# Kernel tuning notes

Hardware: AMD Instinct MI355X
Metric: run time of the kernel (lower is better)

The kernel has to match this reference:

```python
import jax, jax.numpy as jnp
import numpy as np

DIM = 640
HEADS = 10
HEAD_DIM = DIM // HEADS
SCALE = DIM ** (-0.5)  # note: module scales by full dim**-0.5, not head_dim


def setup_inputs() -> dict:
    key = jax.random.key(0)
    ks = jax.random.split(key, 5)
    B, N = 16, 1024
    x = jax.random.normal(ks[0], (B, N, DIM), dtype=jnp.float32)
    w_qkv = jax.random.normal(ks[1], (DIM, 3 * DIM), dtype=jnp.float32) * (DIM ** -0.5)
    b_qkv = jnp.zeros((3 * DIM,), dtype=jnp.float32)
    w_out = jax.random.normal(ks[2], (DIM, DIM), dtype=jnp.float32) * (DIM ** -0.5)
    b_out = jnp.zeros((DIM,), dtype=jnp.float32)
    return {"x": x, "w_qkv": w_qkv, "b_qkv": b_qkv, "w_out": w_out, "b_out": b_out}


def reference(x, w_qkv, b_qkv, w_out, b_out):
    B, N, _ = x.shape
    qkv = x @ w_qkv + b_qkv                     # [B, N, 3*DIM]
    qkv = qkv.reshape(B, N, 3, HEADS, HEAD_DIM)
    q, k, v = qkv[:, :, 0], qkv[:, :, 1], qkv[:, :, 2]   # [B, N, H, Dh]
    # scores: QK^T scaled by dim**-0.5 (module's normfactor)
    scores = jnp.einsum('bihd,bjhd->bhij', q, k) * SCALE  # [B, H, N, N]
    attn = jax.nn.softmax(scores, axis=-1)
    out = jnp.einsum('bhij,bjhd->bihd', attn, v)          # [B, N, H, Dh]
    out = out.reshape(B, N, DIM)
    return out @ w_out + b_out
```

## Files before the change

### kernel.cpp

```cpp
#include <hip/hip_runtime.h>

#define DIM 640
#define NHEADS 10
#define HDIM 64
#define SEQ 1024
#define BATCH 16
#define MROWS (BATCH * SEQ)
#define QKVN (3 * DIM)
#define NBH (BATCH * NHEADS)

typedef float f32x4 __attribute__((ext_vector_type(4)));
typedef __bf16 bf16x8 __attribute__((ext_vector_type(8)));
typedef short s16x4 __attribute__((ext_vector_type(4)));

#define SM_C 0.057027536f

__device__ __forceinline__ unsigned short f2b(float f) {
  union { __bf16 h; unsigned short u; } v;
  v.h = (__bf16)f;
  return v.u;
}

__device__ __forceinline__ f32x4 mfma16(bf16x8 a, bf16x8 b, f32x4 c) {
  return __builtin_amdgcn_mfma_f32_16x16x32_bf16(a, b, c, 0, 0, 0);
}
__device__ __forceinline__ f32x4 mfma1k(s16x4 a, s16x4 b, f32x4 c) {
  return __builtin_amdgcn_mfma_f32_16x16x16bf16_1k(a, b, c, 0, 0, 0);
}

typedef __attribute__((address_space(3))) unsigned int as3_u32;
typedef const __attribute__((address_space(1))) unsigned int as1_u32;
__device__ __forceinline__ void glds16(const unsigned short* g, unsigned short* l) {
  __builtin_amdgcn_global_load_lds((as1_u32*)g, (as3_u32*)l, 16, 0, 0);
}

__global__ __launch_bounds__(256) void convert_x(
    const float* __restrict__ X, unsigned short* __restrict__ xb) {
  int i = (blockIdx.x * 256 + threadIdx.x) * 4;
  float4 v = *(const float4*)(X + i);
  ushort4 s;
  s.x = f2b(v.x); s.y = f2b(v.y); s.z = f2b(v.z); s.w = f2b(v.w);
  *(ushort4*)(xb + i) = s;
}

__global__ __launch_bounds__(256) void transpose_w(
    const float* __restrict__ W, unsigned short* __restrict__ Wt, int R, int C) {
  __shared__ int tile[32][33];
  const int tx = threadIdx.x & 31, ty = threadIdx.x >> 5;
  const int c0 = blockIdx.x * 32, r0 = blockIdx.y * 32;
#pragma unroll
  for (int i = 0; i < 4; ++i)
    tile[ty + 8 * i][tx] = f2b(W[(r0 + ty + 8 * i) * C + c0 + tx]);
  __syncthreads();
#pragma unroll
  for (int i = 0; i < 4; ++i)
    Wt[(c0 + ty + 8 * i) * R + r0 + tx] = (unsigned short)tile[tx][ty + 8 * i];
}

__global__ __launch_bounds__(256) void qkv_gemm(
    const unsigned short* __restrict__ A, const unsigned short* __restrict__ Bt,
    const float* __restrict__ bias,
    unsigned short* __restrict__ qw, unsigned short* __restrict__ kw,
    unsigned short* __restrict__ vtw) {
  __shared__ __attribute__((aligned(16))) unsigned short As[128 * 64];
  __shared__ __attribute__((aligned(16))) unsigned short Bs[128 * 64];
  const int t = threadIdx.x;
  const int lane = t & 63, w = t >> 6;
  const int quad = lane >> 4, cl = lane & 15;
  const int m0 = blockIdx.y * 128, n0 = blockIdx.x * 128;
  const int wr = (w >> 1) * 64, wc = (w & 1) * 64;

  const int r8 = lane >> 3;
  const int sw = ((lane & 7) ^ r8) * 8;
  const unsigned short* asrc = A + (size_t)(m0 + w * 32 + r8) * DIM + sw;
  const unsigned short* bsrc = Bt + (size_t)(n0 + w * 32 + r8) * DIM + sw;

  const int x = cl & 7;
  const int aoff0 = (wr + cl) * 64 + (quad ^ x) * 8;
  const int aoff1 = (wr + cl) * 64 + ((4 + quad) ^ x) * 8;
  const int boff0 = (wc + cl) * 64 + (quad ^ x) * 8;
  const int boff1 = (wc + cl) * 64 + ((4 + quad) ^ x) * 8;

  f32x4 acc[4][4];
#pragma unroll
  for (int i = 0; i < 4; ++i)
#pragma unroll
    for (int j = 0; j < 4; ++j) acc[i][j] = (f32x4){0.f, 0.f, 0.f, 0.f};

  for (int kt = 0; kt < DIM / 64; ++kt) {
    __syncthreads();
#pragma unroll
    for (int i = 0; i < 4; ++i) {
      glds16(asrc + (size_t)i * 8 * DIM, &As[(w * 32 + i * 8) * 64]);
      glds16(bsrc + (size_t)i * 8 * DIM, &Bs[(w * 32 + i * 8) * 64]);
    }
    asrc += 64; bsrc += 64;
    __syncthreads();
#pragma unroll
    for (int ks = 0; ks < 2; ++ks) {
      const int ao = ks ? aoff1 : aoff0, bo = ks ? boff1 : boff0;
      bf16x8 af[4], bfr[4];
#pragma unroll
      for (int i = 0; i < 4; ++i) af[i] = *(const bf16x8*)&As[ao + i * 1024];
#pragma unroll
      for (int j = 0; j < 4; ++j) bfr[j] = *(const bf16x8*)&Bs[bo + j * 1024];
#pragma unroll
      for (int i = 0; i < 4; ++i)
#pragma unroll
        for (int j = 0; j < 4; ++j) acc[i][j] = mfma16(af[i], bfr[j], acc[i][j]);
    }
  }

  const int sec = n0 / DIM;
  unsigned short* qk = (sec == 0) ? qw : kw;
  const float sc = (sec == 0) ? SM_C : 1.0f;
#pragma unroll
  for (int j = 0; j < 4; ++j) {
    int cc = n0 + wc + j * 16 + cl;
    int cr = cc - sec * DIM;
    int h = cr >> 6, d = cr & 63;
    float bv = bias[cc];
#pragma unroll
    for (int i = 0; i < 4; ++i) {
      int rbase = m0 + wr + i * 16 + quad * 4;
      int b = rbase >> 10, n = rbase & 1023;
      int bh = b * NHEADS + h;
      if (sec < 2) {
        size_t base = ((size_t)bh * SEQ + n) * HDIM + d;
#pragma unroll
        for (int r = 0; r < 4; ++r)
          qk[base + (size_t)r * HDIM] = f2b((acc[i][j][r] + bv) * sc);
      } else {
        ushort4 s;
        s.x = f2b(acc[i][j][0] + bv);
        s.y = f2b(acc[i][j][1] + bv);
        s.z = f2b(acc[i][j][2] + bv);
        s.w = f2b(acc[i][j][3] + bv);
        *(ushort4*)(vtw + ((size_t)bh * HDIM + d) * SEQ + n) = s;
      }
    }
  }
}

__global__ __launch_bounds__(256) void attn_kernel(
    const unsigned short* __restrict__ qw, const unsigned short* __restrict__ kw,
    const unsigned short* __restrict__ vtw, unsigned short* __restrict__ out) {
  __shared__ __attribute__((aligned(16))) unsigned short Ks[2][64 * 64];
  __shared__ __attribute__((aligned(16))) unsigned short Vs[2][64 * 64];
  const int t = threadIdx.x;
  const int lane = t & 63, w = t >> 6;
  const int quad = lane >> 4, cl = lane & 15;
  const int flat = blockIdx.x;
  const int bh = flat % NBH;
  const int qb = flat / NBH;
  const size_t qkbase = (size_t)bh * SEQ * HDIM;
  const size_t vbase  = (size_t)bh * HDIM * SEQ;

  const int r8 = lane >> 3;
  const int sw = ((lane & 7) ^ r8) * 8;
  const unsigned short* ksrc = kw + qkbase + (size_t)(w * 16 + r8) * HDIM + sw;
  const unsigned short* vsrc = vtw + vbase + (size_t)(w * 16 + r8) * SEQ + sw;

  const int x = cl & 7;
  const int koff0 = cl * 64 + (quad ^ x) * 8;
  const int koff1 = cl * 64 + ((4 + quad) ^ x) * 8;

  bf16x8 aq[2][2];
#pragma unroll
  for (int i = 0; i < 2; ++i) {
    const unsigned short* qp =
        qw + qkbase + (size_t)(qb * 128 + w * 32 + i * 16 + cl) * HDIM;
    aq[i][0] = *(const bf16x8*)(qp + quad * 8);
    aq[i][1] = *(const bf16x8*)(qp + 32 + quad * 8);
  }

  const s16x4 ones4 = {0x3F80, 0x3F80, 0x3F80, 0x3F80};

  f32x4 o_acc[2][4];
#pragma unroll
  for (int i = 0; i < 2; ++i)
#pragma unroll
    for (int dt = 0; dt < 4; ++dt) o_acc[i][dt] = (f32x4){0.f, 0.f, 0.f, 0.f};
  f32x4 o1[2];
  o1[0] = (f32x4){0.f, 0.f, 0.f, 0.f};
  o1[1] = (f32x4){0.f, 0.f, 0.f, 0.f};

  glds16(ksrc,            &Ks[0][(w * 16) * 64]);
  glds16(ksrc + 8 * HDIM, &Ks[0][(w * 16 + 8) * 64]);
  glds16(vsrc,            &Vs[0][(w * 16) * 64]);
  glds16(vsrc + 8 * SEQ,  &Vs[0][(w * 16 + 8) * 64]);

  for (int kt = 0; kt < 16; ++kt) {
    const int cur = kt & 1, nxt = cur ^ 1;
    __syncthreads();

    if (kt < 15) {
      const unsigned short* kp = ksrc + (size_t)(kt + 1) * 64 * HDIM;
      const unsigned short* vp = vsrc + (kt + 1) * 64;
      glds16(kp,            &Ks[nxt][(w * 16) * 64]);
      glds16(kp + 8 * HDIM, &Ks[nxt][(w * 16 + 8) * 64]);
      glds16(vp,            &Vs[nxt][(w * 16) * 64]);
      glds16(vp + 8 * SEQ,  &Vs[nxt][(w * 16 + 8) * 64]);
    }

    const unsigned short* Kc = &Ks[cur][0];
    const unsigned short* Vc = &Vs[cur][0];

    s16x4 pf[2][4];
#pragma unroll
    for (int jj = 0; jj < 4; ++jj) {
      bf16x8 bk0 = *(const bf16x8*)&Kc[koff0 + jj * 1024];
      bf16x8 bk1 = *(const bf16x8*)&Kc[koff1 + jj * 1024];
#pragma unroll
      for (int i = 0; i < 2; ++i) {
        f32x4 z = (f32x4){0.f, 0.f, 0.f, 0.f};
        z = mfma16(bk0, aq[i][0], z);
        z = mfma16(bk1, aq[i][1], z);
        s16x4 p;
#pragma unroll
        for (int r = 0; r < 4; ++r)
          p[r] = (short)f2b(__builtin_amdgcn_exp2f(z[r]));
        pf[i][jj] = p;
        o1[i] = mfma1k(p, ones4, o1[i]);
      }
    }

#pragma unroll
    for (int dt = 0; dt < 4; ++dt) {
      const int vrow = dt * 16 + cl;
      const int vbase_off = vrow * 64 + (quad & 1) * 4;
      const int vxor = vrow & 7;
#pragma unroll
      for (int jj = 0; jj < 4; ++jj) {
        s16x4 bv = *(const s16x4*)
            &Vc[vbase_off + ((2 * jj + (quad >> 1)) ^ vxor) * 8];
#pragma unroll
        for (int i = 0; i < 2; ++i)
          o_acc[i][dt] = mfma1k(pf[i][jj], bv, o_acc[i][dt]);
      }
    }
  }

  const int b = bh / NHEADS, h = bh % NHEADS;
#pragma unroll
  for (int i = 0; i < 2; ++i)
#pragma unroll
    for (int r = 0; r < 4; ++r) {
      float inv = 1.f / o1[i][r];
      int row = b * SEQ + qb * 128 + w * 32 + i * 16 + quad * 4 + r;
#pragma unroll
      for (int dt = 0; dt < 4; ++dt)
        out[(size_t)row * DIM + h * HDIM + dt * 16 + cl] =
            f2b(o_acc[i][dt][r] * inv);
    }
}

__global__ __launch_bounds__(256) void out_gemm(
    const unsigned short* __restrict__ A, const unsigned short* __restrict__ Bt,
    const float* __restrict__ bias, float* __restrict__ C) {
  __shared__ __attribute__((aligned(16))) unsigned short As[128 * 64];
  __shared__ __attribute__((aligned(16))) unsigned short Bs[128 * 64];
  const int t = threadIdx.x;
  const int lane = t & 63, w = t >> 6;
  const int quad = lane >> 4, cl = lane & 15;
  const int m0 = blockIdx.y * 128, n0 = blockIdx.x * 128;
  const int wr = (w >> 1) * 64, wc = (w & 1) * 64;

  const int r8 = lane >> 3;
  const int sw = ((lane & 7) ^ r8) * 8;
  const unsigned short* asrc = A + (size_t)(m0 + w * 32 + r8) * DIM + sw;
  const unsigned short* bsrc = Bt + (size_t)(n0 + w * 32 + r8) * DIM + sw;

  const int x = cl & 7;
  const int aoff0 = (wr + cl) * 64 + (quad ^ x) * 8;
  const int aoff1 = (wr + cl) * 64 + ((4 + quad) ^ x) * 8;
  const int boff0 = (wc + cl) * 64 + (quad ^ x) * 8;
  const int boff1 = (wc + cl) * 64 + ((4 + quad) ^ x) * 8;

  f32x4 acc[4][4];
#pragma unroll
  for (int i = 0; i < 4; ++i)
#pragma unroll
    for (int j = 0; j < 4; ++j) acc[i][j] = (f32x4){0.f, 0.f, 0.f, 0.f};

  for (int kt = 0; kt < DIM / 64; ++kt) {
    __syncthreads();
#pragma unroll
    for (int i = 0; i < 4; ++i) {
      glds16(asrc + (size_t)i * 8 * DIM, &As[(w * 32 + i * 8) * 64]);
      glds16(bsrc + (size_t)i * 8 * DIM, &Bs[(w * 32 + i * 8) * 64]);
    }
    asrc += 64; bsrc += 64;
    __syncthreads();
#pragma unroll
    for (int ks = 0; ks < 2; ++ks) {
      const int ao = ks ? aoff1 : aoff0, bo = ks ? boff1 : boff0;
      bf16x8 af[4], bfr[4];
#pragma unroll
      for (int i = 0; i < 4; ++i) af[i] = *(const bf16x8*)&As[ao + i * 1024];
#pragma unroll
      for (int j = 0; j < 4; ++j) bfr[j] = *(const bf16x8*)&Bs[bo + j * 1024];
#pragma unroll
      for (int i = 0; i < 4; ++i)
#pragma unroll
        for (int j = 0; j < 4; ++j) acc[i][j] = mfma16(af[i], bfr[j], acc[i][j]);
    }
  }
#pragma unroll
  for (int j = 0; j < 4; ++j) {
    int cc = n0 + wc + j * 16 + cl;
    float bv = bias[cc];
#pragma unroll
    for (int i = 0; i < 4; ++i) {
#pragma unroll
      for (int r = 0; r < 4; ++r) {
        int rr = m0 + wr + i * 16 + quad * 4 + r;
        C[(size_t)rr * DIM + cc] = acc[i][j][r] + bv;
      }
    }
  }
}

extern "C" void kernel_launch(void* const* d_in, const int* in_sizes, int n_in,
                              void* d_out, int out_size, void* d_ws, size_t ws_size,
                              hipStream_t stream) {
  const float* x     = (const float*)d_in[0];
  const float* w_qkv = (const float*)d_in[1];
  const float* b_qkv = (const float*)d_in[2];
  const float* w_out = (const float*)d_in[3];
  const float* b_out = (const float*)d_in[4];
  float* out = (float*)d_out;

  unsigned short* ws = (unsigned short*)d_ws;
  unsigned short* xb      = ws;
  unsigned short* wt_qkv  = ws + 10485760;
  unsigned short* wt_out  = wt_qkv + 1228800;
  unsigned short* qw      = wt_out + 409600;
  unsigned short* kw      = qw + 10485760;
  unsigned short* vtw     = kw + 10485760;
  unsigned short* attn_ws = xb;

  convert_x<<<MROWS * DIM / 1024, 256, 0, stream>>>(x, xb);
  transpose_w<<<dim3(QKVN / 32, DIM / 32), 256, 0, stream>>>(w_qkv, wt_qkv, DIM, QKVN);
  transpose_w<<<dim3(DIM / 32, DIM / 32), 256, 0, stream>>>(w_out, wt_out, DIM, DIM);
  qkv_gemm<<<dim3(QKVN / 128, MROWS / 128), 256, 0, stream>>>(xb, wt_qkv, b_qkv, qw, kw, vtw);
  attn_kernel<<<dim3(NBH * (SEQ / 128)), 256, 0, stream>>>(qw, kw, vtw, attn_ws);
  out_gemm<<<dim3(DIM / 128, MROWS / 128), 256, 0, stream>>>(attn_ws, wt_out, b_out, out);
}
```

Baseline: 256.7 us.

## Merge prep kernels into one launch and read GEMM B-operand directly from global

The x conversion and both weight transposes now run as one launch that branches on block index, removing two kernel launches. Both GEMMs stop staging the weight (B) tile through LDS and instead load the MFMA B fragments straight from global memory each k-step, halving LDS use and the global-to-LDS copies. The cost is uncoalesced, L2-dependent global loads inside the inner loop, which may add latency that the single-buffered loop cannot hide.

```diff
diff --git a/kernel.cpp b/kernel.cpp
--- a/kernel.cpp
+++ b/kernel.cpp
@@ -34,20 +34,32 @@
   __builtin_amdgcn_global_load_lds((as1_u32*)g, (as3_u32*)l, 16, 0, 0);
 }
 
-__global__ __launch_bounds__(256) void convert_x(
-    const float* __restrict__ X, unsigned short* __restrict__ xb) {
-  int i = (blockIdx.x * 256 + threadIdx.x) * 4;
-  float4 v = *(const float4*)(X + i);
-  ushort4 s;
-  s.x = f2b(v.x); s.y = f2b(v.y); s.z = f2b(v.z); s.w = f2b(v.w);
-  *(ushort4*)(xb + i) = s;
-}
-
-__global__ __launch_bounds__(256) void transpose_w(
-    const float* __restrict__ W, unsigned short* __restrict__ Wt, int R, int C) {
+#define NCONV 10240
+#define NT1 1200
+#define NT2 400
+
+__global__ __launch_bounds__(256) void prep_kernel(
+    const float* __restrict__ X, unsigned short* __restrict__ xb,
+    const float* __restrict__ Wq, unsigned short* __restrict__ Wtq,
+    const float* __restrict__ Wo, unsigned short* __restrict__ Wto) {
   __shared__ int tile[32][33];
-  const int tx = threadIdx.x & 31, ty = threadIdx.x >> 5;
-  const int c0 = blockIdx.x * 32, r0 = blockIdx.y * 32;
+  const int b = blockIdx.x, t = threadIdx.x;
+  if (b < NCONV) {
+    int i = (b * 256 + t) * 4;
+    float4 v = *(const float4*)(X + i);
+    ushort4 s;
+    s.x = f2b(v.x); s.y = f2b(v.y); s.z = f2b(v.z); s.w = f2b(v.w);
+    *(ushort4*)(xb + i) = s;
+    return;
+  }
+  const float* W;
+  unsigned short* Wt;
+  int R = DIM, C, bb;
+  if (b < NCONV + NT1) { bb = b - NCONV; W = Wq; Wt = Wtq; C = QKVN; }
+  else                 { bb = b - NCONV - NT1; W = Wo; Wt = Wto; C = DIM; }
+  const int nbx = C / 32;
+  const int c0 = (bb % nbx) * 32, r0 = (bb / nbx) * 32;
+  const int tx = t & 31, ty = t >> 5;
 #pragma unroll
   for (int i = 0; i < 4; ++i)
     tile[ty + 8 * i][tx] = f2b(W[(r0 + ty + 8 * i) * C + c0 + tx]);
@@ -63,7 +75,6 @@
     unsigned short* __restrict__ qw, unsigned short* __restrict__ kw,
     unsigned short* __restrict__ vtw) {
   __shared__ __attribute__((aligned(16))) unsigned short As[128 * 64];
-  __shared__ __attribute__((aligned(16))) unsigned short Bs[128 * 64];
   const int t = threadIdx.x;
   const int lane = t & 63, w = t >> 6;
   const int quad = lane >> 4, cl = lane & 15;
@@ -73,13 +84,12 @@
   const int r8 = lane >> 3;
   const int sw = ((lane & 7) ^ r8) * 8;
   const unsigned short* asrc = A + (size_t)(m0 + w * 32 + r8) * DIM + sw;
-  const unsigned short* bsrc = Bt + (size_t)(n0 + w * 32 + r8) * DIM + sw;
 
   const int x = cl & 7;
   const int aoff0 = (wr + cl) * 64 + (quad ^ x) * 8;
   const int aoff1 = (wr + cl) * 64 + ((4 + quad) ^ x) * 8;
-  const int boff0 = (wc + cl) * 64 + (quad ^ x) * 8;
-  const int boff1 = (wc + cl) * 64 + ((4 + quad) ^ x) * 8;
+
+  const unsigned short* bp0 = Bt + (size_t)(n0 + wc + cl) * DIM + quad * 8;
 
   f32x4 acc[4][4];
 #pragma unroll
@@ -90,20 +100,20 @@
   for (int kt = 0; kt < DIM / 64; ++kt) {
     __syncthreads();
 #pragma unroll
-    for (int i = 0; i < 4; ++i) {
+    for (int i = 0; i < 4; ++i)
       glds16(asrc + (size_t)i * 8 * DIM, &As[(w * 32 + i * 8) * 64]);
-      glds16(bsrc + (size_t)i * 8 * DIM, &Bs[(w * 32 + i * 8) * 64]);
-    }
-    asrc += 64; bsrc += 64;
+    asrc += 64;
     __syncthreads();
 #pragma unroll
     for (int ks = 0; ks < 2; ++ks) {
-      const int ao = ks ? aoff1 : aoff0, bo = ks ? boff1 : boff0;
+      const int ao = ks ? aoff1 : aoff0;
+      const int ko = kt * 64 + ks * 32;
       bf16x8 af[4], bfr[4];
 #pragma unroll
+      for (int j = 0; j < 4; ++j)
+        bfr[j] = *(const bf16x8*)(bp0 + (size_t)j * 16 * DIM + ko);
+#pragma unroll
       for (int i = 0; i < 4; ++i) af[i] = *(const bf16x8*)&As[ao + i * 1024];
-#pragma unroll
-      for (int j = 0; j < 4; ++j) bfr[j] = *(const bf16x8*)&Bs[bo + j * 1024];
 #pragma unroll
       for (int i = 0; i < 4; ++i)
 #pragma unroll
@@ -259,7 +269,6 @@
     const unsigned short* __restrict__ A, const unsigned short* __restrict__ Bt,
     const float* __restrict__ bias, float* __restrict__ C) {
   __shared__ __attribute__((aligned(16))) unsigned short As[128 * 64];
-  __shared__ __attribute__((aligned(16))) unsigned short Bs[128 * 64];
   const int t = threadIdx.x;
   const int lane = t & 63, w = t >> 6;
   const int quad = lane >> 4, cl = lane & 15;
@@ -269,13 +278,12 @@
   const int r8 = lane >> 3;
   const int sw = ((lane & 7) ^ r8) * 8;
   const unsigned short* asrc = A + (size_t)(m0 + w * 32 + r8) * DIM + sw;
-  const unsigned short* bsrc = Bt + (size_t)(n0 + w * 32 + r8) * DIM + sw;
 
   const int x = cl & 7;
   const int aoff0 = (wr + cl) * 64 + (quad ^ x) * 8;
   const int aoff1 = (wr + cl) * 64 + ((4 + quad) ^ x) * 8;
-  const int boff0 = (wc + cl) * 64 + (quad ^ x) * 8;
-  const int boff1 = (wc + cl) * 64 + ((4 + quad) ^ x) * 8;
+
+  const unsigned short* bp0 = Bt + (size_t)(n0 + wc + cl) * DIM + quad * 8;
 
   f32x4 acc[4][4];
 #pragma unroll
@@ -286,20 +294,20 @@
   for (int kt = 0; kt < DIM / 64; ++kt) {
     __syncthreads();
 #pragma unroll
-    for (int i = 0; i < 4; ++i) {
+    for (int i = 0; i < 4; ++i)
       glds16(asrc + (size_t)i * 8 * DIM, &As[(w * 32 + i * 8) * 64]);
-      glds16(bsrc + (size_t)i * 8 * DIM, &Bs[(w * 32 + i * 8) * 64]);
-    }
-    asrc += 64; bsrc += 64;
+    asrc += 64;
     __syncthreads();
 #pragma unroll
     for (int ks = 0; ks < 2; ++ks) {
-      const int ao = ks ? aoff1 : aoff0, bo = ks ? boff1 : boff0;
+      const int ao = ks ? aoff1 : aoff0;
+      const int ko = kt * 64 + ks * 32;
       bf16x8 af[4], bfr[4];
 #pragma unroll
+      for (int j = 0; j < 4; ++j)
+        bfr[j] = *(const bf16x8*)(bp0 + (size_t)j * 16 * DIM + ko);
+#pragma unroll
       for (int i = 0; i < 4; ++i) af[i] = *(const bf16x8*)&As[ao + i * 1024];
-#pragma unroll
-      for (int j = 0; j < 4; ++j) bfr[j] = *(const bf16x8*)&Bs[bo + j * 1024];
 #pragma unroll
       for (int i = 0; i < 4; ++i)
 #pragma unroll
@@ -340,9 +348,7 @@
   unsigned short* vtw     = kw + 10485760;
   unsigned short* attn_ws = xb;
 
-  convert_x<<<MROWS * DIM / 1024, 256, 0, stream>>>(x, xb);
-  transpose_w<<<dim3(QKVN / 32, DIM / 32), 256, 0, stream>>>(w_qkv, wt_qkv, DIM, QKVN);
-  transpose_w<<<dim3(DIM / 32, DIM / 32), 256, 0, stream>>>(w_out, wt_out, DIM, DIM);
+  prep_kernel<<<NCONV + NT1 + NT2, 256, 0, stream>>>(x, xb, w_qkv, wt_qkv, w_out, wt_out);
   qkv_gemm<<<dim3(QKVN / 128, MROWS / 128), 256, 0, stream>>>(xb, wt_qkv, b_qkv, qw, kw, vtw);
   attn_kernel<<<dim3(NBH * (SEQ / 128)), 256, 0, stream>>>(qw, kw, vtw, attn_ws);
   out_gemm<<<dim3(DIM / 128, MROWS / 128), 256, 0, stream>>>(attn_ws, wt_out, b_out, out);
```

New measurement: 314.8 us. +22.7%, slower.
